# Performance work log

Measured on AMD Instinct MI355X. Metric: run time of the kernel, lower is better.

Reference implementation:

```python
import jax, jax.numpy as jnp
import numpy as np

B, V = 1024, 16            # batch, n_variables
NH, SHARE = 32, 4          # n_base_heads, n_heads_sharing_slider
SH = NH // SHARE           # n_slider_heads = 8
D = 128                    # n_token_dim
KV = D * SH                # kv_size = 1024
H = 4096                   # n_hidden


def setup_inputs() -> dict:
    key = jax.random.key(0)
    ks = jax.random.split(key, 14)
    s = 0.02
    inp = {
        "prefix": jax.random.uniform(ks[0], (B, V), jnp.float32, -1.0, 1.0),
        # stacked per-variable key-encoder weights
        "kW1": jax.random.normal(ks[1], (V, KV), jnp.float32) * s,
        "kb1": jnp.zeros((V, KV), jnp.float32),
        "kW2": jax.random.normal(ks[2], (V, KV, H), jnp.float32) * s,
        "kb2": jnp.zeros((V, H), jnp.float32),
        "kW3": jax.random.normal(ks[3], (V, H, KV), jnp.float32) * s,
        "kb3": jnp.zeros((V, KV), jnp.float32),
        # stacked per-variable value-encoder weights
        "vW1": jax.random.normal(ks[4], (V, KV), jnp.float32) * s,
        "vb1": jnp.zeros((V, KV), jnp.float32),
        "vW2": jax.random.normal(ks[5], (V, KV, H), jnp.float32) * s,
        "vb2": jnp.zeros((V, H), jnp.float32),
        "vW3": jax.random.normal(ks[6], (V, H, KV), jnp.float32) * s,
        "vb3": jnp.zeros((V, KV), jnp.float32),
        "attention_factor": jnp.zeros((), jnp.float32),
    }
    return inp


def _mlp(x, W1, b1, W2, b2, W3, b3):
    # x: [B, V] scalar slider per variable; stacked tiny MLPs over V.
    h = jnp.tanh(x[:, :, None] * W1[None] + b1[None])            # [B,V,KV]
    h = jnp.tanh(jnp.einsum('bvk,vkh->bvh', h, W2) + b2[None])   # [B,V,H]
    return jnp.einsum('bvh,vhk->bvk', h, W3) + b3[None]          # [B,V,KV]


def _to_heads(x):
    # [B,V,KV] -> [B, n_base_heads, V, D] with repeat_interleave over slider heads
    x = x.reshape(B, V, SH, D)
    x = jnp.repeat(x, SHARE, axis=2)            # [B,V,NH,D]
    return jnp.transpose(x, (0, 2, 1, 3))       # [B,NH,V,D]


def reference(prefix, kW1, kb1, kW2, kb2, kW3, kb3,
              vW1, vb1, vW2, vb2, vW3, vb3, attention_factor):
    keys = _to_heads(_mlp(prefix, kW1, kb1, kW2, kb2, kW3, kb3))
    values = _to_heads(_mlp(prefix, vW1, vb1, vW2, vb2, vW3, vb3))
    return keys, values, attention_factor
```

## Files before the change

### kernel.cpp

```cpp
#include <hip/hip_runtime.h>
#include <hip/hip_bf16.h>
#include <cstdint>

#define B_   1024
#define V_   16
#define NH_  32
#define SH_  8
#define D_   128
#define KV_  1024
#define H_   4096

typedef __bf16 bf16;
typedef bf16  bf16x8 __attribute__((ext_vector_type(8)));
typedef float f32x2  __attribute__((ext_vector_type(2)));
typedef float f32x4  __attribute__((ext_vector_type(4)));

#define VMCNT(n) asm volatile("s_waitcnt vmcnt(" #n ")" ::: "memory")
#define LGKM0()  asm volatile("s_waitcnt lgkmcnt(0)" ::: "memory")

__device__ __forceinline__ void gl2lds16(const void* g, void* l) {
    __builtin_amdgcn_global_load_lds((const __attribute__((address_space(1))) void*)g,
                                     (__attribute__((address_space(3))) void*)l,
                                     16, 0, 0);
}

__global__ __launch_bounds__(256)
void h1_kernel(const float* __restrict__ prefix, const float* __restrict__ W1,
               const float* __restrict__ b1, bf16* __restrict__ h1)
{
    int gid = blockIdx.x * 256 + threadIdx.x;
    int k8  = gid & 127;
    int b   = (gid >> 7) & 1023;
    int v   = gid >> 17;
    float x = prefix[b * V_ + v];
    const float* wp = W1 + (size_t)v * KV_ + k8 * 8;
    const float* bp = b1 + (size_t)v * KV_ + k8 * 8;
    f32x4 w0 = *(const f32x4*)wp,       w1 = *(const f32x4*)(wp + 4);
    f32x4 q0 = *(const f32x4*)bp,       q1 = *(const f32x4*)(bp + 4);
    bf16x8 o;
#pragma unroll
    for (int j = 0; j < 4; ++j) o[j]     = (bf16)tanhf(fmaf(x, w0[j], q0[j]));
#pragma unroll
    for (int j = 0; j < 4; ++j) o[4 + j] = (bf16)tanhf(fmaf(x, w1[j], q1[j]));
    *(bf16x8*)(h1 + (size_t)gid * 8) = o;
}

template<int MODE, int KDIM, int NDIM>
__global__ __launch_bounds__(512)
void gemm_t2(const bf16* __restrict__ A, const float* __restrict__ Bf,
             const float* __restrict__ bias,
             bf16* __restrict__ outB, float* __restrict__ outF)
{
    __shared__ __align__(16) char smem[131072];

    constexpr int NX  = NDIM / 256;
    constexpr int NXY = NX * 4;
    const int lin = blockIdx.x + NX * blockIdx.y + NXY * blockIdx.z;
    constexpr int NWG = NXY * 16;
    constexpr int CHK = NWG / 8;
    const int swz = (lin & 7) * CHK + (lin >> 3);
    const int v   = swz / NXY;
    const int rem = swz - v * NXY;
    const int m0  = (rem / NX) * 256;
    const int n0  = (rem - (rem / NX) * NX) * 256;

    const int t  = threadIdx.x;
    const int l  = t & 63;
    const int w  = t >> 6;
    const int wr = w >> 2;
    const int wc = w & 3;
    constexpr int NT = KDIM / 64;
    static_assert(NT >= 4, "NT >= 4");

    const bf16*  Av = A  + (size_t)v * 1024 * KDIM + (size_t)m0 * KDIM;
    const float* Bv = Bf + (size_t)v * KDIM * NDIM + n0;

    f32x4 acc[8][4];
#pragma unroll
    for (int i = 0; i < 8; ++i)
#pragma unroll
        for (int j = 0; j < 4; ++j) acc[i][j] = f32x4{0.f, 0.f, 0.f, 0.f};

    const float* bptr = Bv + (size_t)((t >> 7) * 16) * NDIM + 2 * (t & 127);
    f32x2 br[16];

    auto loadBR = [&](int ktile) {
        const float* np = bptr + (size_t)ktile * 64 * NDIM;
#pragma unroll
        for (int j = 0; j < 16; ++j) br[j] = *(const f32x2*)(np + (size_t)j * NDIM);
    };
    auto stageA = [&](int ktile, int ab) {
#pragma unroll
        for (int i = 0; i < 4; ++i) {
            const int off = t + i * 512;
            const int row = off >> 3;
            const int gc  = (off & 7) ^ ((row >> 1) & 7);
            gl2lds16(Av + (size_t)row * KDIM + ktile * 64 + gc * 8,
                     smem + (size_t)ab * 32768 + (size_t)off * 16);
        }
    };
    auto writeB = [&](int bb) {
        bf16* bN = (bf16*)(smem + 65536 + (size_t)bb * 32768);
#pragma unroll
        for (int i = 0; i < 2; ++i)
#pragma unroll
            for (int h = 0; h < 2; ++h) {
                bf16x8 pk;
#pragma unroll
                for (int jj = 0; jj < 8; ++jj) pk[jj] = (bf16)br[h * 8 + jj][i];
                const int n  = 2 * (t & 127) + i;
                const int ch = ((t >> 7) * 2 + h) ^ (t & 7);
                *(bf16x8*)(bN + (size_t)n * 64 + ch * 8) = pk;
            }
    };
    auto mfmaStep = [&](int kt) {
        const bf16* aC = (const bf16*)(smem + (size_t)(kt & 1) * 32768);
        const bf16* bC = (const bf16*)(smem + 65536 + (size_t)(kt & 1) * 32768);
#pragma unroll
        for (int kk = 0; kk < 2; ++kk) {
            bf16x8 af[8], bfv[4];
#pragma unroll
            for (int f = 0; f < 8; ++f) {
                const int mr = wr * 128 + f * 16 + (l & 15);
                const int ca = (kk * 4 + (l >> 4)) ^ ((mr >> 1) & 7);
                af[f] = *(const bf16x8*)(aC + (size_t)mr * 64 + ca * 8);
            }
#pragma unroll
            for (int f = 0; f < 4; ++f) {
                const int nr = wc * 64 + f * 16 + (l & 15);
                const int cb = (kk * 4 + (l >> 4)) ^ ((nr >> 1) & 7);
                bfv[f] = *(const bf16x8*)(bC + (size_t)nr * 64 + cb * 8);
            }
#pragma unroll
            for (int fm = 0; fm < 8; ++fm)
#pragma unroll
                for (int fn = 0; fn < 4; ++fn)
                    acc[fm][fn] = __builtin_amdgcn_mfma_f32_16x16x32_bf16(
                        af[fm], bfv[fn], acc[fm][fn], 0, 0, 0);
        }
    };

    loadBR(0);
    stageA(0, 0);
    VMCNT(4);
    writeB(0);
    VMCNT(0);
    LGKM0();
    __builtin_amdgcn_s_barrier();

    for (int kt = 0; kt < NT - 1; ++kt) {
        loadBR(kt + 1);
        stageA(kt + 1, (kt + 1) & 1);
        mfmaStep(kt);
        VMCNT(4);
        writeB((kt + 1) & 1);
        VMCNT(0);
        LGKM0();
        __builtin_amdgcn_s_barrier();
    }
    mfmaStep(NT - 1);

    const int rbase = (l >> 4) * 4;
    const int cbase = l & 15;
    if (MODE == 0) {
#pragma unroll
        for (int fn = 0; fn < 4; ++fn) {
            const int nc = n0 + wc * 64 + fn * 16 + cbase;
            const float bv = bias[(size_t)v * NDIM + nc];
#pragma unroll
            for (int fm = 0; fm < 8; ++fm)
#pragma unroll
                for (int j = 0; j < 4; ++j) {
                    const int mr = m0 + wr * 128 + fm * 16 + rbase + j;
                    outB[(size_t)v * 1024 * NDIM + (size_t)mr * NDIM + nc] =
                        (bf16)tanhf(acc[fm][fn][j] + bv);
                }
        }
    } else {
        __syncthreads();
        float* scr = (float*)(smem + (size_t)w * 16384);
        const int nb = n0 + wc * 64;
        const int sh = nb >> 7;
        const int db = nb & 127;
#pragma unroll
        for (int p = 0; p < 2; ++p) {
#pragma unroll
            for (int fm = 0; fm < 8; ++fm)
#pragma unroll
                for (int fq = 0; fq < 2; ++fq) {
                    const int fn = 2 * p + fq;
#pragma unroll
                    for (int j = 0; j < 4; ++j) {
                        const int r = fm * 16 + rbase + j;
                        const int c = fq * 16 + cbase;
                        scr[r * 32 + (c ^ (((r >> 2) & 1) << 4))] = acc[fm][fn][j];
                    }
                }
            const int c4   = (l & 7) * 4;
            const int colg = p * 32 + c4;
            f32x4 bv4;
#pragma unroll
            for (int q = 0; q < 4; ++q)
                bv4[q] = bias[(size_t)v * NDIM + nb + colg + q];
#pragma unroll
            for (int i = 0; i < 16; ++i) {
                const int r = i * 8 + (l >> 3);
                f32x4 val = *(const f32x4*)&scr[r * 32 + (c4 ^ (((r >> 2) & 1) << 4))];
#pragma unroll
                for (int q = 0; q < 4; ++q) val[q] += bv4[q];
                const int mr = m0 + wr * 128 + r;
                float* pp = outF + (size_t)mr * (NH_ * V_ * D_)
                                 + (size_t)(sh * 4) * (V_ * D_)
                                 + (size_t)v * D_ + db + colg;
                *(f32x4*)(pp)               = val;
                *(f32x4*)(pp + V_ * D_)     = val;
                *(f32x4*)(pp + 2 * V_ * D_) = val;
                *(f32x4*)(pp + 3 * V_ * D_) = val;
            }
        }
    }
}

__global__ void tail_kernel(const float* __restrict__ af, float* __restrict__ out)
{
    out[0] = af[0];
}

extern "C" void kernel_launch(void* const* d_in, const int* in_sizes, int n_in,
                              void* d_out, int out_size, void* d_ws, size_t ws_size,
                              hipStream_t stream)
{
    const float* prefix = (const float*)d_in[0];
    const float* W1[2]  = {(const float*)d_in[1], (const float*)d_in[7]};
    const float* b1[2]  = {(const float*)d_in[2], (const float*)d_in[8]};
    const float* W2[2]  = {(const float*)d_in[3], (const float*)d_in[9]};
    const float* b2[2]  = {(const float*)d_in[4], (const float*)d_in[10]};
    const float* W3[2]  = {(const float*)d_in[5], (const float*)d_in[11]};
    const float* b3[2]  = {(const float*)d_in[6], (const float*)d_in[12]};
    const float* afac   = (const float*)d_in[13];

    bf16* h1 = (bf16*)d_ws;
    bf16* h2 = (bf16*)((char*)d_ws + (size_t)33554432);
    float* outp = (float*)d_out;

    for (int m = 0; m < 2; ++m) {
        h1_kernel<<<8192, 256, 0, stream>>>(prefix, W1[m], b1[m], h1);
        gemm_t2<0, 1024, 4096><<<dim3(16, 4, 16), 512, 0, stream>>>(
            h1, W2[m], b2[m], h2, nullptr);
        gemm_t2<1, 4096, 1024><<<dim3(4, 4, 16), 512, 0, stream>>>(
            h2, W3[m], b3[m], nullptr, outp + (size_t)m * (B_ * NH_ * V_ * D_));
    }
    tail_kernel<<<1, 1, 0, stream>>>(afac, outp + (size_t)2 * B_ * NH_ * V_ * D_);
}
```

Measured before the change: 913.4 us.

## Batch key and value MLPs into single launches and use nontemporal output stores

Merges the key and value encoder passes so each stage (h1, GEMM2, GEMM3) launches once, with twice the workgroups and a model index picking weights, biases and outputs. Separate h2 buffers are allocated for the two models in the workspace. The final GEMM's replicated output writes become nontemporal stores to avoid polluting cache. This removes launch gaps and tail underutilization, especially for the GEMM3 grid of 256 workgroups, at the cost of more workspace memory.

Result: no change. 913.8 us (+0.0%).

```diff
diff --git a/kernel.cpp b/kernel.cpp
--- a/kernel.cpp
+++ b/kernel.cpp
@@ -25,13 +25,18 @@
 }
 
 __global__ __launch_bounds__(256)
-void h1_kernel(const float* __restrict__ prefix, const float* __restrict__ W1,
-               const float* __restrict__ b1, bf16* __restrict__ h1)
+void h1_kernel(const float* __restrict__ prefix,
+               const float* __restrict__ W1a, const float* __restrict__ b1a,
+               const float* __restrict__ W1b, const float* __restrict__ b1b,
+               bf16* __restrict__ h1)
 {
     int gid = blockIdx.x * 256 + threadIdx.x;
     int k8  = gid & 127;
     int b   = (gid >> 7) & 1023;
-    int v   = gid >> 17;
+    int vm  = gid >> 17;
+    int v   = vm & 15;
+    const float* W1 = (vm >> 4) ? W1b : W1a;
+    const float* b1 = (vm >> 4) ? b1b : b1a;
     float x = prefix[b * V_ + v];
     const float* wp = W1 + (size_t)v * KV_ + k8 * 8;
     const float* bp = b1 + (size_t)v * KV_ + k8 * 8;
@@ -47,22 +52,31 @@
 
 template<int MODE, int KDIM, int NDIM>
 __global__ __launch_bounds__(512)
-void gemm_t2(const bf16* __restrict__ A, const float* __restrict__ Bf,
-             const float* __restrict__ bias,
-             bf16* __restrict__ outB, float* __restrict__ outF)
+void gemm_t2(const bf16* __restrict__ A0, const bf16* __restrict__ A1,
+             const float* __restrict__ Bf0, const float* __restrict__ Bf1,
+             const float* __restrict__ bias0, const float* __restrict__ bias1,
+             bf16* __restrict__ outB0, bf16* __restrict__ outB1,
+             float* __restrict__ outF)
 {
     __shared__ __align__(16) char smem[131072];
 
     constexpr int NX  = NDIM / 256;
-    constexpr int NXY = NX * 4;
+    constexpr int NMB = 4;
+    constexpr int NXY = NX * NMB;
     const int lin = blockIdx.x + NX * blockIdx.y + NXY * blockIdx.z;
-    constexpr int NWG = NXY * 16;
+    constexpr int NWG = NXY * 32;
     constexpr int CHK = NWG / 8;
     const int swz = (lin & 7) * CHK + (lin >> 3);
-    const int v   = swz / NXY;
-    const int rem = swz - v * NXY;
+    const int mm  = swz / (NXY * 16);
+    const int r2  = swz - mm * (NXY * 16);
+    const int v   = r2 / NXY;
+    const int rem = r2 - v * NXY;
     const int m0  = (rem / NX) * 256;
     const int n0  = (rem - (rem / NX) * NX) * 256;
+
+    const bf16*  Abase = mm ? A1 : A0;
+    const float* Bbase = mm ? Bf1 : Bf0;
+    const float* bias  = mm ? bias1 : bias0;
 
     const int t  = threadIdx.x;
     const int l  = t & 63;
@@ -72,8 +86,8 @@
     constexpr int NT = KDIM / 64;
     static_assert(NT >= 4, "NT >= 4");
 
-    const bf16*  Av = A  + (size_t)v * 1024 * KDIM + (size_t)m0 * KDIM;
-    const float* Bv = Bf + (size_t)v * KDIM * NDIM + n0;
+    const bf16*  Av = Abase + (size_t)v * 1024 * KDIM + (size_t)m0 * KDIM;
+    const float* Bv = Bbase + (size_t)v * KDIM * NDIM + n0;
 
     f32x4 acc[8][4];
 #pragma unroll
@@ -163,6 +177,7 @@
     const int rbase = (l >> 4) * 4;
     const int cbase = l & 15;
     if (MODE == 0) {
+        bf16* outB = mm ? outB1 : outB0;
 #pragma unroll
         for (int fn = 0; fn < 4; ++fn) {
             const int nc = n0 + wc * 64 + fn * 16 + cbase;
@@ -177,6 +192,7 @@
                 }
         }
     } else {
+        float* outm = outF + (size_t)mm * ((size_t)B_ * NH_ * V_ * D_);
         __syncthreads();
         float* scr = (float*)(smem + (size_t)w * 16384);
         const int nb = n0 + wc * 64;
@@ -209,13 +225,13 @@
 #pragma unroll
                 for (int q = 0; q < 4; ++q) val[q] += bv4[q];
                 const int mr = m0 + wr * 128 + r;
-                float* pp = outF + (size_t)mr * (NH_ * V_ * D_)
+                float* pp = outm + (size_t)mr * (NH_ * V_ * D_)
                                  + (size_t)(sh * 4) * (V_ * D_)
                                  + (size_t)v * D_ + db + colg;
-                *(f32x4*)(pp)               = val;
-                *(f32x4*)(pp + V_ * D_)     = val;
-                *(f32x4*)(pp + 2 * V_ * D_) = val;
-                *(f32x4*)(pp + 3 * V_ * D_) = val;
+                __builtin_nontemporal_store(val, (f32x4*)(pp));
+                __builtin_nontemporal_store(val, (f32x4*)(pp + V_ * D_));
+                __builtin_nontemporal_store(val, (f32x4*)(pp + 2 * V_ * D_));
+                __builtin_nontemporal_store(val, (f32x4*)(pp + 3 * V_ * D_));
             }
         }
     }
@@ -239,16 +255,17 @@
     const float* b3[2]  = {(const float*)d_in[6], (const float*)d_in[12]};
     const float* afac   = (const float*)d_in[13];
 
-    bf16* h1 = (bf16*)d_ws;
-    bf16* h2 = (bf16*)((char*)d_ws + (size_t)33554432);
+    bf16* h1  = (bf16*)d_ws;
+    bf16* h2a = (bf16*)((char*)d_ws + (size_t)67108864);
+    bf16* h2b = (bf16*)((char*)d_ws + (size_t)67108864 + (size_t)134217728);
     float* outp = (float*)d_out;
 
-    for (int m = 0; m < 2; ++m) {
-        h1_kernel<<<8192, 256, 0, stream>>>(prefix, W1[m], b1[m], h1);
-        gemm_t2<0, 1024, 4096><<<dim3(16, 4, 16), 512, 0, stream>>>(
-            h1, W2[m], b2[m], h2, nullptr);
-        gemm_t2<1, 4096, 1024><<<dim3(4, 4, 16), 512, 0, stream>>>(
-            h2, W3[m], b3[m], nullptr, outp + (size_t)m * (B_ * NH_ * V_ * D_));
-    }
+    h1_kernel<<<16384, 256, 0, stream>>>(prefix, W1[0], b1[0], W1[1], b1[1], h1);
+    gemm_t2<0, 1024, 4096><<<dim3(16, 4, 32), 512, 0, stream>>>(
+        h1, h1 + (size_t)16777216, W2[0], W2[1], b2[0], b2[1],
+        h2a, h2b, nullptr);
+    gemm_t2<1, 4096, 1024><<<dim3(4, 4, 32), 512, 0, stream>>>(
+        h2a, h2b, W3[0], W3[1], b3[0], b3[1],
+        nullptr, nullptr, outp);
     tail_kernel<<<1, 1, 0, stream>>>(afac, outp + (size_t)2 * B_ * NH_ * V_ * D_);
 }
```
